# Performance work log

Hardware: AMD Instinct MI355X
Metric: run time of the kernel (lower is better)

## Reference

```python
import jax, jax.numpy as jnp
import numpy as np

V_WORDS = 100000
N_BLOCKS = 32
D = 256                      # embedding_dim == block_dim
VOCAB = V_WORDS + N_BLOCKS   # 100032
S_LEN = 64                   # max_story_len
Q_LEN = 16                   # max_query_len
N_SENT = 2048                # sentences per story (scan length)
N_Q = 128                    # number of queries


def prelu(x, a):
    return jnp.where(x >= 0, x, a * x)


def setup_inputs() -> dict:
    key = jax.random.key(0)
    ks = jax.random.split(key, 12)
    emb = jax.random.normal(ks[0], (VOCAB, D), jnp.float32) * 0.02
    inp = {
        "inputs": jax.random.randint(ks[1], (N_SENT, S_LEN), 0, VOCAB),
        "query": jax.random.randint(ks[2], (N_Q, Q_LEN), 0, VOCAB),
        "h0": jax.random.uniform(ks[3], (N_BLOCKS * D,), jnp.float32),
        "emb": emb,
        "f_story": jax.random.normal(ks[4], (S_LEN, D), jnp.float32) * 0.1 + 1.0,
        "f_query": jax.random.normal(ks[5], (Q_LEN, D), jnp.float32) * 0.1 + 1.0,
        "U": jax.random.normal(ks[6], (D, D), jnp.float32) * 0.05,
        "V": jax.random.normal(ks[7], (D, D), jnp.float32) * 0.05,
        "W": jax.random.normal(ks[8], (D, D), jnp.float32) * 0.05,
        "bias": jnp.full((D,), 0.001, jnp.float32),
        "keys": emb[VOCAB - N_BLOCKS:],           # memory keys = last n_blocks embedding rows
        "a_mem": jnp.asarray(0.25, jnp.float32),  # PReLU slope (memory cell)
        "Hw": jax.random.normal(ks[9], (D, D), jnp.float32) * 0.05,
        "Hb": jnp.full((D,), 0.001, jnp.float32),
        "Rw": jax.random.normal(ks[10], (VOCAB, D), jnp.float32) * 0.05,
        "Rb": jnp.full((VOCAB,), 0.001, jnp.float32),
        "a_out": jnp.asarray(0.25, jnp.float32),   # PReLU slope (output module)
    }
    return inp


def reference(inputs, query, h0, emb, f_story, f_query, U, V, W, bias, keys,
              a_mem, Hw, Hb, Rw, Rb, a_out):
    # Input/query encoders: sum over positions of embedding * positional mask f
    x = jnp.sum(emb[inputs] * f_story, axis=1)   # [N_SENT, D]
    q = jnp.sum(emb[query] * f_query, axis=1)    # [N_Q, D]

    H0 = h0.reshape(N_BLOCKS, D)

    def step(H, s):
        # gate: sigmoid(<s,hj> + <s,key_j>) per block
        g = jax.nn.sigmoid(H @ s + keys @ s)                       # [N_BLOCKS]
        # candidate: PReLU(U hj + V key_j + W s + b)
        hs = prelu(H @ U.T + keys @ V.T + (W @ s)[None, :] + bias, a_mem)
        Hn = H + g[:, None] * hs
        Hn = Hn / jnp.linalg.norm(Hn, axis=-1, keepdims=True)      # per-block L2 norm
        return Hn, None

    Hf, _ = jax.lax.scan(step, H0, x)            # sequential memory updates

    # Output module: u_i = sum_j log_softmax(q_i * h_j) * h_j
    lsm = jax.nn.log_softmax(q[:, None, :] * Hf[None, :, :], axis=-1)  # [N_Q, N_BLOCKS, D]
    u = jnp.sum(lsm * Hf[None, :, :], axis=1)                          # [N_Q, D]
    y = prelu(q + u @ Hw.T + Hb, a_out) @ Rw.T + Rb                    # [N_Q, VOCAB]
    return y, Hf.reshape(-1)
```

## Files before the change

### kernel.cpp

```cpp
#include <hip/hip_runtime.h>
#include <hip/hip_bf16.h>

#define N_SENT 2048
#define S_LEN  64
#define QL     16
#define NQ     128
#define NB     32
#define DD     256
#define VOCAB  100032

#define PADC 264

using bf16x8 = __attribute__((ext_vector_type(8))) short;
using f32x4  = __attribute__((ext_vector_type(4))) float;

#define WS_X   0
#define WS_WX  (WS_X  + N_SENT*DD)
#define WS_Q   (WS_WX + N_SENT*DD)
#define WS_KS  (WS_Q  + NQ*DD)
#define WS_KVB (WS_KS + N_SENT*NB)
#define WS_HF  (WS_KVB+ NB*DD)
#define WS_Z   (WS_HF + NB*DD)
#define WS_BF  (WS_Z  + NQ*DD)

__global__ __launch_bounds__(256) void encode_story(
    const int* __restrict__ inp, const float* __restrict__ emb,
    const float* __restrict__ f, float* __restrict__ X)
{
    const int t = blockIdx.x, d = threadIdx.x;
    __shared__ int idx[S_LEN];
    if (d < S_LEN) idx[d] = inp[t*S_LEN + d];
    __syncthreads();
    float acc = 0.f;
#pragma unroll 4
    for (int p = 0; p < S_LEN; ++p)
        acc += emb[(size_t)idx[p]*DD + d] * f[p*DD + d];
    X[t*DD + d] = acc;
}

__global__ __launch_bounds__(256) void encode_query(
    const int* __restrict__ qry, const float* __restrict__ emb,
    const float* __restrict__ f, float* __restrict__ Q)
{
    const int i = blockIdx.x, d = threadIdx.x;
    __shared__ int idx[QL];
    if (d < QL) idx[d] = qry[i*QL + d];
    __syncthreads();
    float acc = 0.f;
#pragma unroll
    for (int p = 0; p < QL; ++p)
        acc += emb[(size_t)idx[p]*DD + d] * f[p*DD + d];
    Q[i*DD + d] = acc;
}

__global__ __launch_bounds__(256) void wx_ks(
    const float* __restrict__ X, const float* __restrict__ W,
    const float* __restrict__ keys, float* __restrict__ WX, float* __restrict__ KS)
{
    const int t = blockIdx.x, n = threadIdx.x;
    __shared__ float xs[DD];
    xs[n] = X[t*DD + n];
    __syncthreads();
    float acc = 0.f;
    const float4* wr = (const float4*)&W[n*DD];
    const float4* xp = (const float4*)xs;
#pragma unroll 8
    for (int k4 = 0; k4 < 64; ++k4) {
        float4 w = wr[k4], x = xp[k4];
        acc += w.x*x.x + w.y*x.y + w.z*x.z + w.w*x.w;
    }
    WX[t*DD + n] = acc;
    if (n < NB) {
        float a2 = 0.f;
        const float4* kr = (const float4*)&keys[n*DD];
#pragma unroll 8
        for (int k4 = 0; k4 < 64; ++k4) {
            float4 kv = kr[k4], x = xp[k4];
            a2 += kv.x*x.x + kv.y*x.y + kv.z*x.z + kv.w*x.w;
        }
        KS[t*NB + n] = a2;
    }
}

__global__ __launch_bounds__(256) void kvb_kernel(
    const float* __restrict__ keys, const float* __restrict__ V,
    const float* __restrict__ bias, float* __restrict__ KVB)
{
    const int jj = blockIdx.x, n = threadIdx.x;
    __shared__ float ks[DD];
    ks[n] = keys[jj*DD + n];
    __syncthreads();
    float acc = bias[n];
    const float4* vr = (const float4*)&V[n*DD];
    const float4* kp = (const float4*)ks;
#pragma unroll 8
    for (int k4 = 0; k4 < 64; ++k4) {
        float4 v = vr[k4], k = kp[k4];
        acc += v.x*k.x + v.y*k.y + v.z*k.z + v.w*k.w;
    }
    KVB[jj*DD + n] = acc;
}

__global__ __launch_bounds__(64) void prep_ufrag(
    const float* __restrict__ U, ushort* __restrict__ Bf)
{
    const int f = blockIdx.x;
    const int l = threadIdx.x;
    const int kt = f & 7, nt = f >> 3;
    const int n  = nt*16 + (l & 15);
    const int kb = kt*32 + (l >> 4)*8;
    ushort out[8];
#pragma unroll
    for (int i = 0; i < 8; ++i) {
        __hip_bfloat16 b = __float2bfloat16(U[n*DD + kb + i]);
        out[i] = *reinterpret_cast<ushort*>(&b);
    }
    *(uint4*)&Bf[((size_t)f*64 + l)*8] = *(const uint4*)out;
}

__device__ __forceinline__ void split_hilo(float v, ushort& hi, ushort& lo)
{
    unsigned b = __float_as_uint(v);
    unsigned h = b & 0xFFFF0000u;
    hi = (ushort)(h >> 16);
    lo = (ushort)(__float_as_uint(v - __uint_as_float(h)) >> 16);
}

template <int CTRL>
__device__ __forceinline__ int dpp_i(int v) {
    return __builtin_amdgcn_update_dpp(0, v, CTRL, 0xF, 0xF, true);
}
template <int CTRL>
__device__ __forceinline__ float dpp_f(float x) {
    return __int_as_float(dpp_i<CTRL>(__float_as_int(x)));
}

__device__ __forceinline__ float red16(float x) {
    x += dpp_f<0xB1>(x);
    x += dpp_f<0x4E>(x);
    x += dpp_f<0x141>(x);
    x += dpp_f<0x140>(x);
    return x;
}
__device__ __forceinline__ float red8(float x) {
    x += dpp_f<0xB1>(x);
    x += dpp_f<0x4E>(x);
    x += dpp_f<0x141>(x);
    return x;
}

#define SCAN_STEP(WXU0, WXU1, XU0, XU1, KSU, CURB, T)                          \
  {                                                                            \
    const int nxtb = (CURB) ^ 1;                                               \
    float2 pv = pred[(CURB)][lane & 7];                                        \
    float rn = red8(pv.x), rg = red8(pv.y);                                    \
    const float inv  = rsqrtf(rn);                                             \
    const float gate = __builtin_amdgcn_rcpf(1.f + __expf(-(inv*rg + (KSU)))); \
    if (c15 < 2) {                                                             \
      _Pragma("unroll")                                                        \
      for (int kt = 0; kt < 8; ++kt)                                           \
        a[kt] = *(const bf16x8*)&arr[(CURB)][c15][kt*32 + g*8];                \
    }                                                                          \
    f32x4 q[2][2];                                                             \
    _Pragma("unroll")                                                          \
    for (int tau = 0; tau < 2; ++tau)                                          \
      _Pragma("unroll")                                                        \
      for (int kh = 0; kh < 2; ++kh)                                           \
        q[tau][kh] = (f32x4){0.f, 0.f, 0.f, 0.f};                              \
    _Pragma("unroll")                                                          \
    for (int ki = 0; ki < 4; ++ki) {                                           \
      q[0][0] = __builtin_amdgcn_mfma_f32_16x16x32_bf16(a[ki],     bU[0][ki],     q[0][0], 0, 0, 0); \
      q[1][0] = __builtin_amdgcn_mfma_f32_16x16x32_bf16(a[ki],     bU[1][ki],     q[1][0], 0, 0, 0); \
      q[0][1] = __builtin_amdgcn_mfma_f32_16x16x32_bf16(a[ki + 4], bU[0][ki + 4], q[0][1], 0, 0, 0); \
      q[1][1] = __builtin_amdgcn_mfma_f32_16x16x32_bf16(a[ki + 4], bU[1][ki + 4], q[1][1], 0, 0, 0); \
    }                                                                          \
    if (own) {                                                                 \
      float ns = 0.f, gs = 0.f;                                                \
      _Pragma("unroll")                                                        \
      for (int tau = 0; tau < 2; ++tau) {                                      \
        const float xnt = tau ? (XU1) : (XU0);                                 \
        const float wxt = tau ? (WXU1) : (WXU0);                               \
        float ymm = (q[tau][0][0] + q[tau][1][0])                              \
                  + (q[tau][0][1] + q[tau][1][1]);                             \
        float y  = inv*ymm + kv[tau] + wxt;                                    \
        float hs = (y >= 0.f) ? y : am*y;                                      \
        float hn = inv*h[tau] + gate*hs;                                       \
        h[tau] = hn;                                                           \
        ns += hn*hn;  gs += hn*xnt;                                            \
        ushort hh, hl; split_hilo(hn, hh, hl);                                 \
        int hh2 = dpp_i<0xB1>((int)hh);                                        \
        int hl2 = dpp_i<0xB1>((int)hl);                                        \
        if (evn) {                                                             \
          uint ph = (uint)hh | ((uint)(ushort)hh2 << 16);                      \
          uint pl = (uint)hl | ((uint)(ushort)hl2 << 16);                      \
          const int ucol = 16*w + 8*tau + (c15 >> 1);                          \
          ((uint*)&arr[nxtb][0][0])[ucol] = ph;                                \
          ((uint*)&arr[nxtb][1][0])[ucol] = pl;                                \
        }                                                                      \
      }                                                                        \
      ns = red16(ns);  gs = red16(gs);                                         \
      if (lane == 0) pred[nxtb][w] = make_float2(ns, gs);                      \
    }                                                                          \
    {                                                                          \
      const int tw = ((T) + 4 < N_SENT) ? (T) + 4 : N_SENT - 1;                \
      const int tx = ((T) + 5 < N_SENT) ? (T) + 5 : N_SENT - 1;                \
      if (own) {                                                               \
        WXU0 = WX[tw*DD + col0];  WXU1 = WX[tw*DD + col1];                     \
        XU0  = X [tx*DD + col0];  XU1  = X [tx*DD + col1];                     \
      }                                                                        \
      KSU = KS[tw*NB + j];                                                     \
    }                                                                          \
    asm volatile("s_waitcnt lgkmcnt(0)" ::: "memory");                         \
    __builtin_amdgcn_sched_barrier(0);                                         \
    __builtin_amdgcn_s_barrier();                                              \
    __builtin_amdgcn_sched_barrier(0);                                         \
  }

__global__ __launch_bounds__(512)
__attribute__((amdgpu_waves_per_eu(2, 2)))
void scan_kernel(
    const float* __restrict__ X,  const float* __restrict__ WX,
    const float* __restrict__ KS, const float* __restrict__ KVB,
    const ushort* __restrict__ Bf, const float* __restrict__ h0,
    const float* __restrict__ a_mem_p, float* __restrict__ Hf,
    float* __restrict__ HfOut)
{
    const int j    = blockIdx.x;
    const int tid  = threadIdx.x;
    const int w    = tid >> 6;
    const int lane = tid & 63;
    const int c15  = lane & 15;
    const int g    = lane >> 4;
    const bool own = (g == 0);
    const bool evn = !(c15 & 1);

    __shared__ __align__(16) ushort arr[2][2][PADC];
    __shared__ float2 pred[2][8];

    bf16x8 bU[2][8];
#pragma unroll
    for (int tau = 0; tau < 2; ++tau)
#pragma unroll
        for (int kt = 0; kt < 8; ++kt)
            bU[tau][kt] = *(const bf16x8*)
                &Bf[(((size_t)(2*w + tau)*8 + kt)*64 + lane)*8];

    const float am = *a_mem_p;
    const int col0 = 32*w + c15, col1 = col0 + 16;

    float h[2] = {0.f, 0.f}, kv[2] = {0.f, 0.f};
    float gsi = 0.f;
    if (own) {
#pragma unroll
        for (int tau = 0; tau < 2; ++tau) {
            const int ct = tau ? col1 : col0;
            h[tau]  = h0[j*DD + ct];
            kv[tau] = KVB[j*DD + ct];
            gsi += h[tau] * X[ct];
            ushort hh, hl; split_hilo(h[tau], hh, hl);
            arr[0][0][ct] = hh;  arr[0][1][ct] = hl;
        }
        gsi = red16(gsi);
    }
    if (lane == 0) pred[0][w] = make_float2(0.125f, gsi);

    float wx00=0,wx01=0,x00=0,x01=0, wx10=0,wx11=0,x10=0,x11=0;
    float wx20=0,wx21=0,x20=0,x21=0, wx30=0,wx31=0,x30=0,x31=0;
    if (own) {
        wx00 = WX[       col0]; wx01 = WX[       col1];
        wx10 = WX[  DD + col0]; wx11 = WX[  DD + col1];
        wx20 = WX[2*DD + col0]; wx21 = WX[2*DD + col1];
        wx30 = WX[3*DD + col0]; wx31 = WX[3*DD + col1];
        x00  = X [  DD + col0]; x01  = X [  DD + col1];
        x10  = X [2*DD + col0]; x11  = X [2*DD + col1];
        x20  = X [3*DD + col0]; x21  = X [3*DD + col1];
        x30  = X [4*DD + col0]; x31  = X [4*DD + col1];
    }
    float ks0 = KS[j], ks1 = KS[NB + j], ks2 = KS[2*NB + j], ks3 = KS[3*NB + j];
    __syncthreads();

    bf16x8 a[8];
#pragma unroll
    for (int kt = 0; kt < 8; ++kt) a[kt] = (bf16x8){0,0,0,0,0,0,0,0};

    for (int tb = 0; tb < N_SENT; tb += 4) {
        SCAN_STEP(wx00, wx01, x00, x01, ks0, 0, tb + 0);
        SCAN_STEP(wx10, wx11, x10, x11, ks1, 1, tb + 1);
        SCAN_STEP(wx20, wx21, x20, x21, ks2, 0, tb + 2);
        SCAN_STEP(wx30, wx31, x30, x31, ks3, 1, tb + 3);
    }

    {
        float2 pv = pred[0][lane & 7];
        const float inv = rsqrtf(red8(pv.x));
        if (own) {
#pragma unroll
            for (int tau = 0; tau < 2; ++tau) {
                const int ct = tau ? col1 : col0;
                const float v = h[tau] * inv;
                Hf[j*DD + ct]    = v;
                HfOut[j*DD + ct] = v;
            }
        }
    }
}

__global__ __launch_bounds__(256) void out_small(
    const float* __restrict__ Qe, const float* __restrict__ Hfm,
    const float* __restrict__ Hw, const float* __restrict__ Hb,
    const float* __restrict__ a_out_p, float* __restrict__ Z)
{
    const int i = blockIdx.x, d = threadIdx.x;
    __shared__ float hsh[NB*DD];
    __shared__ float red[4];
    __shared__ float csh[NB];
    __shared__ float ush[DD];
#pragma unroll
    for (int jj = 0; jj < NB; ++jj) hsh[jj*DD + d] = Hfm[jj*DD + d];
    const float qd = Qe[i*DD + d];
    __syncthreads();
    float s2 = 0.f;
#pragma unroll
    for (int jj = 0; jj < NB; ++jj) { float h = hsh[jj*DD + d]; s2 += h*h; }
    for (int jj = 0; jj < NB; ++jj) {
        float p = qd * hsh[jj*DD + d];
        float m = p;
#pragma unroll
        for (int o = 32; o; o >>= 1) m = fmaxf(m, __shfl_xor(m, o));
        if ((d & 63) == 0) red[d >> 6] = m;
        __syncthreads();
        m = fmaxf(fmaxf(red[0], red[1]), fmaxf(red[2], red[3]));
        __syncthreads();
        float e = expf(p - m);
#pragma unroll
        for (int o = 32; o; o >>= 1) e += __shfl_xor(e, o);
        if ((d & 63) == 0) red[d >> 6] = e;
        __syncthreads();
        if (d == 0) csh[jj] = m + logf(red[0] + red[1] + red[2] + red[3]);
        __syncthreads();
    }
    float u = qd * s2;
#pragma unroll
    for (int jj = 0; jj < NB; ++jj) u -= csh[jj] * hsh[jj*DD + d];
    ush[d] = u;
    __syncthreads();
    float acc = qd + Hb[d];
    const float4* hwr = (const float4*)&Hw[d*DD];
    const float4* up  = (const float4*)ush;
#pragma unroll 8
    for (int k4 = 0; k4 < 64; ++k4) {
        float4 w = hwr[k4], uu = up[k4];
        acc += w.x*uu.x + w.y*uu.y + w.z*uu.z + w.w*uu.w;
    }
    const float ao = *a_out_p;
    Z[i*DD + d] = (acc >= 0.f) ? acc : ao * acc;
}

__global__ __launch_bounds__(256) void out_gemm(
    const float* __restrict__ Z, const float* __restrict__ Rw,
    const float* __restrict__ Rb, float* __restrict__ Y)
{
    const int vt  = blockIdx.x * 64;
    const int tid = threadIdx.x;
    __shared__ float rw_sh[64*DD];
    __shared__ float z_sh[64*DD];
#pragma unroll
    for (int it = 0; it < 16; ++it) {
        int f = tid + it*256;
        int row = f >> 6, c = f & 63;
        float4 v = *(const float4*)&Rw[(size_t)(vt + row)*DD + 4*c];
        int u = c ^ ((row >> 2) & 7);
        *(float4*)&rw_sh[row*DD + 4*u] = v;
    }
    const int vg = tid & 15;
    const int ig = tid >> 4;
    const float4 rb4 = *(const float4*)&Rb[vt + vg*4];

    for (int ic = 0; ic < 2; ++ic) {
        const int i0 = ic * 64;
        __syncthreads();
#pragma unroll
        for (int it = 0; it < 16; ++it) {
            int f = tid + it*256;
            int row = f >> 6, c = f & 63;
            float4 v = *(const float4*)&Z[(i0 + row)*DD + 4*c];
            int u = c ^ ((row >> 2) & 7);
            *(float4*)&z_sh[row*DD + 4*u] = v;
        }
        __syncthreads();
        float acc[4][4];
#pragma unroll
        for (int b = 0; b < 4; ++b)
#pragma unroll
            for (int a = 0; a < 4; ++a) acc[b][a] = 0.f;
#pragma unroll 2
        for (int kc = 0; kc < 64; ++kc) {
            float4 ra[4], zb[4];
            const int ur = (kc ^ (vg & 7)) * 4;
            const int uz = (kc ^ (ig & 7)) * 4;
#pragma unroll
            for (int a = 0; a < 4; ++a) ra[a] = *(const float4*)&rw_sh[(vg*4 + a)*DD + ur];
#pragma unroll
            for (int b = 0; b < 4; ++b) zb[b] = *(const float4*)&z_sh[(ig*4 + b)*DD + uz];
#pragma unroll
            for (int b = 0; b < 4; ++b)
#pragma unroll
                for (int a = 0; a < 4; ++a)
                    acc[b][a] += zb[b].x*ra[a].x + zb[b].y*ra[a].y
                               + zb[b].z*ra[a].z + zb[b].w*ra[a].w;
        }
#pragma unroll
        for (int b = 0; b < 4; ++b) {
            int i = i0 + ig*4 + b;
            float4 o;
            o.x = acc[b][0] + rb4.x; o.y = acc[b][1] + rb4.y;
            o.z = acc[b][2] + rb4.z; o.w = acc[b][3] + rb4.w;
            *(float4*)&Y[(size_t)i*VOCAB + vt + vg*4] = o;
        }
    }
}

extern "C" void kernel_launch(void* const* d_in, const int* in_sizes, int n_in,
                              void* d_out, int out_size, void* d_ws, size_t ws_size,
                              hipStream_t stream)
{
    (void)in_sizes; (void)n_in; (void)out_size; (void)ws_size;
    const int*   inputs  = (const int*)  d_in[0];
    const int*   query   = (const int*)  d_in[1];
    const float* h0      = (const float*)d_in[2];
    const float* emb     = (const float*)d_in[3];
    const float* f_story = (const float*)d_in[4];
    const float* f_query = (const float*)d_in[5];
    const float* U       = (const float*)d_in[6];
    const float* V       = (const float*)d_in[7];
    const float* W       = (const float*)d_in[8];
    const float* bias    = (const float*)d_in[9];
    const float* keys    = (const float*)d_in[10];
    const float* a_mem   = (const float*)d_in[11];
    const float* Hw      = (const float*)d_in[12];
    const float* Hb      = (const float*)d_in[13];
    const float* Rw      = (const float*)d_in[14];
    const float* Rb      = (const float*)d_in[15];
    const float* a_out   = (const float*)d_in[16];

    float* ws  = (float*)d_ws;
    float* X   = ws + WS_X;
    float* WX  = ws + WS_WX;
    float* Qe  = ws + WS_Q;
    float* KS  = ws + WS_KS;
    float* KVB = ws + WS_KVB;
    float* Hf  = ws + WS_HF;
    float* Z   = ws + WS_Z;
    ushort* Bf = (ushort*)(ws + WS_BF);

    float* Y     = (float*)d_out;
    float* HfOut = Y + (size_t)NQ * VOCAB;

    encode_story<<<N_SENT, 256, 0, stream>>>(inputs, emb, f_story, X);
    encode_query<<<NQ,    256, 0, stream>>>(query,  emb, f_query, Qe);
    wx_ks      <<<N_SENT, 256, 0, stream>>>(X, W, keys, WX, KS);
    kvb_kernel <<<NB,     256, 0, stream>>>(keys, V, bias, KVB);
    prep_ufrag <<<128,     64, 0, stream>>>(U, Bf);
    scan_kernel<<<NB,     512, 0, stream>>>(X, WX, KS, KVB, Bf, h0, a_mem, Hf, HfOut);
    out_small  <<<NQ,     256, 0, stream>>>(Qe, Hf, Hw, Hb, a_out, Z);
    out_gemm   <<<VOCAB/64, 256, 0, stream>>>(Z, Rw, Rb, Y);
}
```

Before: 1.820 ms.

## Halve scan workgroup to 4 waves, each owning 64 output columns

The sequential scan kernel now runs 4 waves of 256 threads per block instead of 8, and each wave computes four 16-column tiles of the U product instead of two. The cross-wave reduction of the norm and gate partial sums shrinks from 8 to 4 entries, and barriers synchronise fewer waves. The aim is to cut per-step barrier and reduction latency on the serial critical path. In exchange each wave issues twice as many MFMAs per step and holds twice as many U fragments in registers, so per-step compute latency per wave grows.

```diff
diff --git a/kernel.cpp b/kernel.cpp
--- a/kernel.cpp
+++ b/kernel.cpp
@@ -14,14 +14,14 @@
 using bf16x8 = __attribute__((ext_vector_type(8))) short;
 using f32x4  = __attribute__((ext_vector_type(4))) float;
 
-#define WS_X   0
-#define WS_WX  (WS_X  + N_SENT*DD)
-#define WS_Q   (WS_WX + N_SENT*DD)
-#define WS_KS  (WS_Q  + NQ*DD)
-#define WS_KVB (WS_KS + N_SENT*NB)
-#define WS_HF  (WS_KVB+ NB*DD)
-#define WS_Z   (WS_HF + NB*DD)
-#define WS_BF  (WS_Z  + NQ*DD)
+#define WS_X    0
+#define WS_WX   (WS_X  + N_SENT*DD)
+#define WS_Q    (WS_WX + N_SENT*DD)
+#define WS_KS   (WS_Q  + NQ*DD)
+#define WS_KVB  (WS_KS + N_SENT*NB)
+#define WS_HF   (WS_KVB+ NB*DD)
+#define WS_Z    (WS_HF + NB*DD)
+#define WS_BF   (WS_Z  + NQ*DD)
 
 __global__ __launch_bounds__(256) void encode_story(
     const int* __restrict__ inp, const float* __restrict__ emb,
@@ -142,18 +142,19 @@
     x += dpp_f<0x140>(x);
     return x;
 }
-__device__ __forceinline__ float red8(float x) {
+__device__ __forceinline__ float red4(float x) {
     x += dpp_f<0xB1>(x);
     x += dpp_f<0x4E>(x);
-    x += dpp_f<0x141>(x);
     return x;
 }
 
-#define SCAN_STEP(WXU0, WXU1, XU0, XU1, KSU, CURB, T)                          \
+#define CSEL(V, TAU) ((TAU)==0 ? (V).x : (TAU)==1 ? (V).y : (TAU)==2 ? (V).z : (V).w)
+
+#define SCAN_STEP(WXQ, XQ, KSU, CURB, T)                                       \
   {                                                                            \
     const int nxtb = (CURB) ^ 1;                                               \
-    float2 pv = pred[(CURB)][lane & 7];                                        \
-    float rn = red8(pv.x), rg = red8(pv.y);                                    \
+    float2 pv = pred[(CURB)][lane & 3];                                        \
+    float rn = red4(pv.x), rg = red4(pv.y);                                    \
     const float inv  = rsqrtf(rn);                                             \
     const float gate = __builtin_amdgcn_rcpf(1.f + __expf(-(inv*rg + (KSU)))); \
     if (c15 < 2) {                                                             \
@@ -161,25 +162,26 @@
       for (int kt = 0; kt < 8; ++kt)                                           \
         a[kt] = *(const bf16x8*)&arr[(CURB)][c15][kt*32 + g*8];                \
     }                                                                          \
-    f32x4 q[2][2];                                                             \
+    f32x4 q[4][2];                                                             \
     _Pragma("unroll")                                                          \
-    for (int tau = 0; tau < 2; ++tau)                                          \
+    for (int tl = 0; tl < 4; ++tl)                                             \
       _Pragma("unroll")                                                        \
       for (int kh = 0; kh < 2; ++kh)                                           \
-        q[tau][kh] = (f32x4){0.f, 0.f, 0.f, 0.f};                              \
+        q[tl][kh] = (f32x4){0.f, 0.f, 0.f, 0.f};                               \
     _Pragma("unroll")                                                          \
     for (int ki = 0; ki < 4; ++ki) {                                           \
-      q[0][0] = __builtin_amdgcn_mfma_f32_16x16x32_bf16(a[ki],     bU[0][ki],     q[0][0], 0, 0, 0); \
-      q[1][0] = __builtin_amdgcn_mfma_f32_16x16x32_bf16(a[ki],     bU[1][ki],     q[1][0], 0, 0, 0); \
-      q[0][1] = __builtin_amdgcn_mfma_f32_16x16x32_bf16(a[ki + 4], bU[0][ki + 4], q[0][1], 0, 0, 0); \
-      q[1][1] = __builtin_amdgcn_mfma_f32_16x16x32_bf16(a[ki + 4], bU[1][ki + 4], q[1][1], 0, 0, 0); \
+      _Pragma("unroll")                                                        \
+      for (int tl = 0; tl < 4; ++tl) {                                         \
+        q[tl][0] = __builtin_amdgcn_mfma_f32_16x16x32_bf16(a[ki],     bU[tl][ki],     q[tl][0], 0, 0, 0); \
+        q[tl][1] = __builtin_amdgcn_mfma_f32_16x16x32_bf16(a[ki + 4], bU[tl][ki + 4], q[tl][1], 0, 0, 0); \
+      }                                                                        \
     }                                                                          \
     if (own) {                                                                 \
       float ns = 0.f, gs = 0.f;                                                \
       _Pragma("unroll")                                                        \
-      for (int tau = 0; tau < 2; ++tau) {                                      \
-        const float xnt = tau ? (XU1) : (XU0);                                 \
-        const float wxt = tau ? (WXU1) : (WXU0);                               \
+      for (int tau = 0; tau < 4; ++tau) {                                      \
+        const float xnt = CSEL(XQ, tau);                                       \
+        const float wxt = CSEL(WXQ, tau);                                      \
         float ymm = (q[tau][0][0] + q[tau][1][0])                              \
                   + (q[tau][0][1] + q[tau][1][1]);                             \
         float y  = inv*ymm + kv[tau] + wxt;                                    \
@@ -193,7 +195,7 @@
         if (evn) {                                                             \
           uint ph = (uint)hh | ((uint)(ushort)hh2 << 16);                      \
           uint pl = (uint)hl | ((uint)(ushort)hl2 << 16);                      \
-          const int ucol = 16*w + 8*tau + (c15 >> 1);                          \
+          const int ucol = 32*w + 8*tau + (c15 >> 1);                          \
           ((uint*)&arr[nxtb][0][0])[ucol] = ph;                                \
           ((uint*)&arr[nxtb][1][0])[ucol] = pl;                                \
         }                                                                      \
@@ -205,8 +207,10 @@
       const int tw = ((T) + 4 < N_SENT) ? (T) + 4 : N_SENT - 1;                \
       const int tx = ((T) + 5 < N_SENT) ? (T) + 5 : N_SENT - 1;                \
       if (own) {                                                               \
-        WXU0 = WX[tw*DD + col0];  WXU1 = WX[tw*DD + col1];                     \
-        XU0  = X [tx*DD + col0];  XU1  = X [tx*DD + col1];                     \
+        WXQ.x = WX[tw*DD + col0]; WXQ.y = WX[tw*DD + col1];                    \
+        WXQ.z = WX[tw*DD + col2]; WXQ.w = WX[tw*DD + col3];                    \
+        XQ.x  = X [tx*DD + col0]; XQ.y  = X [tx*DD + col1];                    \
+        XQ.z  = X [tx*DD + col2]; XQ.w  = X [tx*DD + col3];                    \
       }                                                                        \
       KSU = KS[tw*NB + j];                                                     \
     }                                                                          \
@@ -216,8 +220,8 @@
     __builtin_amdgcn_sched_barrier(0);                                         \
   }
 
-__global__ __launch_bounds__(512)
-__attribute__((amdgpu_waves_per_eu(2, 2)))
+__global__ __launch_bounds__(256)
+__attribute__((amdgpu_waves_per_eu(1, 1)))
 void scan_kernel(
     const float* __restrict__ X,  const float* __restrict__ WX,
     const float* __restrict__ KS, const float* __restrict__ KVB,
@@ -235,25 +239,26 @@
     const bool evn = !(c15 & 1);
 
     __shared__ __align__(16) ushort arr[2][2][PADC];
-    __shared__ float2 pred[2][8];
-
-    bf16x8 bU[2][8];
-#pragma unroll
-    for (int tau = 0; tau < 2; ++tau)
+    __shared__ float2 pred[2][4];
+
+    bf16x8 bU[4][8];
+#pragma unroll
+    for (int tl = 0; tl < 4; ++tl)
 #pragma unroll
         for (int kt = 0; kt < 8; ++kt)
-            bU[tau][kt] = *(const bf16x8*)
-                &Bf[(((size_t)(2*w + tau)*8 + kt)*64 + lane)*8];
+            bU[tl][kt] = *(const bf16x8*)
+                &Bf[(((size_t)(4*w + tl)*8 + kt)*64 + lane)*8];
 
     const float am = *a_mem_p;
-    const int col0 = 32*w + c15, col1 = col0 + 16;
-
-    float h[2] = {0.f, 0.f}, kv[2] = {0.f, 0.f};
+    const int col0 = 64*w + c15,  col1 = col0 + 16;
+    const int col2 = col0 + 32,   col3 = col0 + 48;
+
+    float h[4] = {0.f,0.f,0.f,0.f}, kv[4] = {0.f,0.f,0.f,0.f};
     float gsi = 0.f;
     if (own) {
 #pragma unroll
-        for (int tau = 0; tau < 2; ++tau) {
-            const int ct = tau ? col1 : col0;
+        for (int tau = 0; tau < 4; ++tau) {
+            const int ct = col0 + 16*tau;
             h[tau]  = h0[j*DD + ct];
             kv[tau] = KVB[j*DD + ct];
             gsi += h[tau] * X[ct];
@@ -262,19 +267,19 @@
         }
         gsi = red16(gsi);
     }
-    if (lane == 0) pred[0][w] = make_float2(0.125f, gsi);
-
-    float wx00=0,wx01=0,x00=0,x01=0, wx10=0,wx11=0,x10=0,x11=0;
-    float wx20=0,wx21=0,x20=0,x21=0, wx30=0,wx31=0,x30=0,x31=0;
+    if (lane == 0) pred[0][w] = make_float2(0.25f, gsi);
+
+    float4 wxq0 = {0,0,0,0}, wxq1 = {0,0,0,0}, wxq2 = {0,0,0,0}, wxq3 = {0,0,0,0};
+    float4 xq0  = {0,0,0,0}, xq1  = {0,0,0,0}, xq2  = {0,0,0,0}, xq3  = {0,0,0,0};
     if (own) {
-        wx00 = WX[       col0]; wx01 = WX[       col1];
-        wx10 = WX[  DD + col0]; wx11 = WX[  DD + col1];
-        wx20 = WX[2*DD + col0]; wx21 = WX[2*DD + col1];
-        wx30 = WX[3*DD + col0]; wx31 = WX[3*DD + col1];
-        x00  = X [  DD + col0]; x01  = X [  DD + col1];
-        x10  = X [2*DD + col0]; x11  = X [2*DD + col1];
-        x20  = X [3*DD + col0]; x21  = X [3*DD + col1];
-        x30  = X [4*DD + col0]; x31  = X [4*DD + col1];
+        wxq0 = make_float4(WX[col0],       WX[col1],       WX[col2],       WX[col3]);
+        wxq1 = make_float4(WX[DD+col0],    WX[DD+col1],    WX[DD+col2],    WX[DD+col3]);
+        wxq2 = make_float4(WX[2*DD+col0],  WX[2*DD+col1],  WX[2*DD+col2],  WX[2*DD+col3]);
+        wxq3 = make_float4(WX[3*DD+col0],  WX[3*DD+col1],  WX[3*DD+col2],  WX[3*DD+col3]);
+        xq0  = make_float4(X[DD+col0],     X[DD+col1],     X[DD+col2],     X[DD+col3]);
+        xq1  = make_float4(X[2*DD+col0],   X[2*DD+col1],   X[2*DD+col2],   X[2*DD+col3]);
+        xq2  = make_float4(X[3*DD+col0],   X[3*DD+col1],   X[3*DD+col2],   X[3*DD+col3]);
+        xq3  = make_float4(X[4*DD+col0],   X[4*DD+col1],   X[4*DD+col2],   X[4*DD+col3]);
     }
     float ks0 = KS[j], ks1 = KS[NB + j], ks2 = KS[2*NB + j], ks3 = KS[3*NB + j];
     __syncthreads();
@@ -284,19 +289,19 @@
     for (int kt = 0; kt < 8; ++kt) a[kt] = (bf16x8){0,0,0,0,0,0,0,0};
 
     for (int tb = 0; tb < N_SENT; tb += 4) {
-        SCAN_STEP(wx00, wx01, x00, x01, ks0, 0, tb + 0);
-        SCAN_STEP(wx10, wx11, x10, x11, ks1, 1, tb + 1);
-        SCAN_STEP(wx20, wx21, x20, x21, ks2, 0, tb + 2);
-        SCAN_STEP(wx30, wx31, x30, x31, ks3, 1, tb + 3);
+        SCAN_STEP(wxq0, xq0, ks0, 0, tb + 0);
+        SCAN_STEP(wxq1, xq1, ks1, 1, tb + 1);
+        SCAN_STEP(wxq2, xq2, ks2, 0, tb + 2);
+        SCAN_STEP(wxq3, xq3, ks3, 1, tb + 3);
     }
 
     {
-        float2 pv = pred[0][lane & 7];
-        const float inv = rsqrtf(red8(pv.x));
+        float2 pv = pred[0][lane & 3];
+        const float inv = rsqrtf(red4(pv.x));
         if (own) {
 #pragma unroll
-            for (int tau = 0; tau < 2; ++tau) {
-                const int ct = tau ? col1 : col0;
+            for (int tau = 0; tau < 4; ++tau) {
+                const int ct = col0 + 16*tau;
                 const float v = h[tau] * inv;
                 Hf[j*DD + ct]    = v;
                 HfOut[j*DD + ct] = v;
@@ -461,7 +466,7 @@
     wx_ks      <<<N_SENT, 256, 0, stream>>>(X, W, keys, WX, KS);
     kvb_kernel <<<NB,     256, 0, stream>>>(keys, V, bias, KVB);
     prep_ufrag <<<128,     64, 0, stream>>>(U, Bf);
-    scan_kernel<<<NB,     512, 0, stream>>>(X, WX, KS, KVB, Bf, h0, a_mem, Hf, HfOut);
+    scan_kernel<<<NB,     256, 0, stream>>>(X, WX, KS, KVB, Bf, h0, a_mem, Hf, HfOut);
     out_small  <<<NQ,     256, 0, stream>>>(Qe, Hf, Hw, Hb, a_out, Z);
     out_gemm   <<<VOCAB/64, 256, 0, stream>>>(Z, Rw, Rb, Y);
 }
```

After: 2.175 ms. 19.5% more time.
